# Kernel optimization log

Hardware: AMD Instinct MI355X
Metric: run time of the kernel (lower is better)

The kernel has to match this reference:

```python
import jax, jax.numpy as jnp
import numpy as np

B, N_IMG, D = 256, 128, 768
E, S, H = 3, 44, 1024  # S = ceil(128/3) rounded up to multiple of 4; H = 4*D//E
MAX_SLOTS = 88
LN_EPS = 1e-5


def setup_inputs() -> dict:
    key = jax.random.key(0)
    ks = jax.random.split(key, 12)
    x = jax.random.normal(ks[0], (B, N_IMG + 1, D), dtype=jnp.float32)
    attn_weight = jax.random.uniform(ks[1], (B, N_IMG), dtype=jnp.float32)
    ln_gamma = jnp.ones((D,), jnp.float32)
    ln_beta = jnp.zeros((D,), jnp.float32)
    vsg_w = jax.random.normal(ks[2], (D + 1, D), jnp.float32) / np.sqrt(D + 1)
    vsg_b = jnp.zeros((D,), jnp.float32)
    mu = jax.random.normal(ks[3], (E, D, MAX_SLOTS), jnp.float32) / np.sqrt(D)
    scale = jnp.ones((1,), jnp.float32)
    # per-expert MLP: kaiming-ish / xavier-ish random params
    w1 = jax.random.normal(ks[4], (E, D, H), jnp.float32) * np.sqrt(2.0 / D)
    b1 = jnp.zeros((E, H), jnp.float32)
    w2 = jax.random.normal(ks[5], (E, H, D), jnp.float32) * np.sqrt(2.0 / (H + D))
    b2 = jnp.zeros((E, D), jnp.float32)
    cw1 = jax.random.normal(ks[6], (D, 4 * D), jnp.float32) * np.sqrt(2.0 / D)
    cb1 = jnp.zeros((4 * D,), jnp.float32)
    cw2 = jax.random.normal(ks[7], (4 * D, D), jnp.float32) * np.sqrt(2.0 / (4 * D))
    cb2 = jnp.zeros((D,), jnp.float32)
    return dict(x=x, attn_weight=attn_weight, ln_gamma=ln_gamma, ln_beta=ln_beta,
                vsg_w=vsg_w, vsg_b=vsg_b, mu=mu, scale=scale,
                w1=w1, b1=b1, w2=w2, b2=b2, cw1=cw1, cb1=cb1, cw2=cw2, cb2=cb2)


def reference(x, attn_weight, ln_gamma, ln_beta, vsg_w, vsg_b, mu, scale,
              w1, b1, w2, b2, cw1, cb1, cw2, cb2):
    b, np1, d = x.shape
    n = np1 - 1
    img = x[:, 1:, :]            # [B, N, D]
    cls = x[:, 0, :]             # [B, D]

    # LayerNorm on image tokens
    mean = img.mean(-1, keepdims=True)
    var = img.var(-1, keepdims=True)  # biased, matches torch LayerNorm
    img_n = (img - mean) * jax.lax.rsqrt(var + LN_EPS) * ln_gamma + ln_beta

    # slot bias from [cls_feat, mean attention] -> visible_slot_gen (mode='original')
    attn_feat = attn_weight.mean(axis=1, keepdims=True)            # [B, 1]
    slot_input = jnp.concatenate([cls, attn_feat], axis=-1)        # [B, D+1]
    slot_bias = slot_input @ vsg_w + vsg_b                         # [B, D]

    # adjusted slot prototypes: mu[:, :, :S].permute(1,0,2) + slot_bias broadcast over (E, S)
    adj_mu = mu[:, :, :S].transpose(1, 0, 2)[None] + slot_bias[:, :, None, None]  # [B, D, E, S]

    logits = jnp.einsum('bnd,bdes->bnes', img_n * scale, adj_mu)   # [B, N, E, S]

    # expert group mask from attention thresholds (groups (1,1,1))
    vis = attn_weight > 0.7
    part = (attn_weight >= 0.3) & (attn_weight <= 0.7)
    occ = attn_weight < 0.3
    emask = jnp.stack([vis, part, occ], axis=-1).astype(logits.dtype)  # [B, N, E]
    logits = logits * emask[:, :, :, None]

    # softmax over tokens (dispatch) and over flattened slots (combine)
    dispatch = jax.nn.softmax(logits, axis=1)                      # [B, N, E, S]
    combine = jax.nn.softmax(logits.reshape(b, n, E * S), axis=-1) # [B, N, E*S]

    slot_in = jnp.einsum('bnd,bnes->besd', img, dispatch)          # [B, E, S, D]

    # batched per-expert MLP (fused grouped GEMM instead of python loop)
    h = jax.nn.gelu(jnp.einsum('besd,edh->besh', slot_in, w1) + b1[:, None, :],
                    approximate=False)
    slot_out = jnp.einsum('besh,ehd->besd', h, w2) + b2[:, None, :]  # [B, E, S, D]

    slot_flat = slot_out.reshape(b, E * S, d)
    img_out = jnp.einsum('bsd,bns->bnd', slot_flat, combine)       # [B, N, D]

    # CLS token through its dedicated dense MLP
    cls_h = jax.nn.gelu(cls @ cw1 + cb1, approximate=False)
    cls_out = cls_h @ cw2 + cb2                                    # [B, D]

    return jnp.concatenate([cls_out[:, None, :], img_out], axis=1)  # [B, N+1, D]
```

## Files before the change

kernel.cpp:

```cpp
#include <hip/hip_runtime.h>
#include <hip/hip_bf16.h>
#include <math.h>

#define NB   256
#define NIMG 128
#define DIM  768
#define NE   3
#define NS   44
#define NH   1024
#define ESL  132
#define NTOK (NB*NIMG)
#define MAXSLOTS 88
#define BIGI (1 << 30)
#define KPAD 160

typedef __bf16 bf16x8 __attribute__((ext_vector_type(8)));
typedef float f32x4 __attribute__((ext_vector_type(4)));
typedef const __attribute__((address_space(1))) void* gas_t;
typedef __attribute__((address_space(3))) void* las_t;

__device__ __forceinline__ float gelu_f(float v) {
    return 0.5f * v * (1.0f + erff(v * 0.70710678118654752f));
}

__device__ __forceinline__ float block_reduce_sum256(float v, float* red) {
    int tid = threadIdx.x;
    red[tid] = v;
    __syncthreads();
    for (int s = 128; s > 0; s >>= 1) {
        if (tid < s) red[tid] += red[tid + s];
        __syncthreads();
    }
    float r = red[0];
    __syncthreads();
    return r;
}

__global__ void repack_mu_k(const float* __restrict__ mu, __hip_bfloat16* __restrict__ bt) {
    int idx = blockIdx.x * 256 + threadIdx.x;
    if (idx >= 256 * DIM) return;
    int r = idx / DIM, d = idx - r * DIM;
    float v = 0.f;
    if (r < ESL) {
        int e = r / NS, s = r - e * NS;
        v = mu[((size_t)e * DIM + d) * MAXSLOTS + s];
    }
    bt[idx] = __float2bfloat16(v);
}

__global__ void transpose_bf16_k(const float* __restrict__ in, __hip_bfloat16* __restrict__ outp,
                                 int R, int Cc, long long inBS, long long outBS) {
    __shared__ float t[32][33];
    in   += (long long)blockIdx.z * inBS;
    outp += (long long)blockIdx.z * outBS;
    int c0 = blockIdx.x * 32, r0 = blockIdx.y * 32;
    int tx = threadIdx.x, ty = threadIdx.y;
    for (int i = 0; i < 32; i += 8) {
        int r = r0 + ty + i, c = c0 + tx;
        t[ty + i][tx] = (r < R && c < Cc) ? in[(size_t)r * Cc + c] : 0.f;
    }
    __syncthreads();
    for (int i = 0; i < 32; i += 8) {
        int r = c0 + ty + i, c = r0 + tx;
        if (r < Cc && c < R) outp[(size_t)r * R + c] = __float2bfloat16(t[tx][ty + i]);
    }
}

__global__ void cls_bf16_k(const float* __restrict__ x, __hip_bfloat16* __restrict__ cls16) {
    int idx = blockIdx.x * 256 + threadIdx.x;
    if (idx >= NB * DIM) return;
    int b = idx / DIM, j = idx - b * DIM;
    cls16[idx] = __float2bfloat16(x[(size_t)b * 129 * DIM + j]);
}

__global__ void zero_pad_k(__hip_bfloat16* __restrict__ p) {
    const int per = KPAD - ESL;
    const int total = NB * DIM * per;
    int idx = blockIdx.x * 256 + threadIdx.x;
    if (idx >= total) return;
    int bd = idx / per, k = idx - bd * per;
    p[(size_t)bd * KPAD + ESL + k] = __float2bfloat16(0.f);
}

__global__ void slot_bias_k(const float* __restrict__ x, const float* __restrict__ aw,
                            const float* __restrict__ vsg_w, const float* __restrict__ vsg_b,
                            float* __restrict__ slot_bias) {
    __shared__ float red[256];
    __shared__ float cls[DIM];
    int b = blockIdx.x, tid = threadIdx.x;
    float a = (tid < NIMG) ? aw[b * NIMG + tid] : 0.f;
    float af = block_reduce_sum256(a, red) * (1.0f / NIMG);
    for (int j = tid; j < DIM; j += 256) cls[j] = x[(size_t)b * 129 * DIM + j];
    __syncthreads();
    int j0 = tid, j1 = tid + 256, j2 = tid + 512;
    float acc0 = 0.f, acc1 = 0.f, acc2 = 0.f;
    for (int d = 0; d < DIM; ++d) {
        float c = cls[d];
        const float* wr = vsg_w + (size_t)d * DIM;
        acc0 = fmaf(c, wr[j0], acc0);
        acc1 = fmaf(c, wr[j1], acc1);
        acc2 = fmaf(c, wr[j2], acc2);
    }
    const float* wl = vsg_w + (size_t)DIM * DIM;
    float* out = slot_bias + (size_t)b * DIM;
    out[j0] = acc0 + vsg_b[j0] + af * wl[j0];
    out[j1] = acc1 + vsg_b[j1] + af * wl[j1];
    out[j2] = acc2 + vsg_b[j2] + af * wl[j2];
}

__global__ void ln_t2_k(const float* __restrict__ x, const float* __restrict__ gamma,
                        const float* __restrict__ beta, const float* __restrict__ slot_bias,
                        __hip_bfloat16* __restrict__ img_n, float* __restrict__ t2) {
    __shared__ float red[256];
    int tok = blockIdx.x;
    int b = tok >> 7, n = tok & 127;
    int tid = threadIdx.x;
    const float* row = x + ((size_t)b * 129 + 1 + n) * DIM;
    float v0 = row[tid], v1 = row[tid + 256], v2 = row[tid + 512];
    float s  = block_reduce_sum256(v0 + v1 + v2, red);
    float ss = block_reduce_sum256(v0*v0 + v1*v1 + v2*v2, red);
    float mean = s * (1.0f / DIM);
    float var  = ss * (1.0f / DIM) - mean * mean;
    float inv  = rsqrtf(var + 1e-5f);
    const float* sb = slot_bias + (size_t)b * DIM;
    __hip_bfloat16* orow = img_n + (size_t)tok * DIM;
    float tacc = 0.f;
    int j = tid;
    float y0 = (v0 - mean) * inv * gamma[j] + beta[j]; orow[j] = __float2bfloat16(y0); tacc = fmaf(y0, sb[j], tacc);
    j = tid + 256;
    float y1 = (v1 - mean) * inv * gamma[j] + beta[j]; orow[j] = __float2bfloat16(y1); tacc = fmaf(y1, sb[j], tacc);
    j = tid + 512;
    float y2 = (v2 - mean) * inv * gamma[j] + beta[j]; orow[j] = __float2bfloat16(y2); tacc = fmaf(y2, sb[j], tacc);
    float t = block_reduce_sum256(tacc, red);
    if (tid == 0) t2[tok] = t;
}

__global__ void mask_k(float* __restrict__ L, const float* __restrict__ t2,
                       const float* __restrict__ aw, const float* __restrict__ scale) {
    int idx = blockIdx.x * 256 + threadIdx.x;
    if (idx >= NTOK * ESL) return;
    int tok = idx / ESL, r = idx - tok * ESL;
    int e = r / NS;
    float a = aw[tok];
    int sel = (a > 0.7f) ? 0 : ((a >= 0.3f) ? 1 : 2);
    float v = 0.f;
    if (e == sel) v = scale[0] * (L[idx] + t2[tok]);
    L[idx] = v;
}

__global__ void dispatch_k(const float* __restrict__ L, __hip_bfloat16* __restrict__ dT16) {
    __shared__ float red[128];
    int es = blockIdx.x, b = blockIdx.y, tid = threadIdx.x;
    float v = L[((size_t)(b * NIMG + tid)) * ESL + es];
    red[tid] = v; __syncthreads();
    for (int s = 64; s > 0; s >>= 1) { if (tid < s) red[tid] = fmaxf(red[tid], red[tid + s]); __syncthreads(); }
    float mx = red[0]; __syncthreads();
    float e = __expf(v - mx);
    red[tid] = e; __syncthreads();
    for (int s = 64; s > 0; s >>= 1) { if (tid < s) red[tid] += red[tid + s]; __syncthreads(); }
    float sum = red[0];
    dT16[((size_t)b * ESL + es) * NIMG + tid] = __float2bfloat16(e / sum);
}

__global__ void combine_k(const float* __restrict__ L, __hip_bfloat16* __restrict__ C) {
    int tok = blockIdx.x, lane = threadIdx.x;
    const float* row = L + (size_t)tok * ESL;
    float v0 = row[lane], v1 = row[lane + 64];
    bool has2 = lane < (ESL - 128);
    float v2 = has2 ? row[lane + 128] : -1e30f;
    float m = fmaxf(fmaxf(v0, v1), v2);
    for (int o = 32; o > 0; o >>= 1) m = fmaxf(m, __shfl_xor(m, o));
    float e0 = __expf(v0 - m), e1 = __expf(v1 - m);
    float e2 = has2 ? __expf(v2 - m) : 0.f;
    float s = e0 + e1 + e2;
    for (int o = 32; o > 0; o >>= 1) s += __shfl_xor(s, o);
    float inv = 1.0f / s;
    __hip_bfloat16* orow = C + (size_t)tok * KPAD;
    orow[lane] = __float2bfloat16(e0 * inv);
    orow[lane + 64] = __float2bfloat16(e1 * inv);
    if (has2) orow[lane + 128] = __float2bfloat16(e2 * inv);
    else if (lane < KPAD - 128) orow[lane + 128] = __float2bfloat16(0.f);
}

__global__ __launch_bounds__(256)
void mfma2_k(const __hip_bfloat16* __restrict__ A_, long long aBS, int lda, int Mrows,
             const __hip_bfloat16* __restrict__ Bt_, long long bBS, int ldb, int Nrows,
             const float* __restrict__ bias, long long biasBS,
             void* __restrict__ Cv, long long cBS, int ldc, int cSub, long long cOuter,
             int Mlim, int Nlim, int K, int act, int out_bf16, int ctrans)
{
    const unsigned short* A  = (const unsigned short*)A_  + (long long)blockIdx.z * aBS;
    const unsigned short* Bt = (const unsigned short*)Bt_ + (long long)blockIdx.z * bBS;
    if (bias) bias += (long long)blockIdx.z * biasBS;
    long long cbase = (long long)blockIdx.z * cBS;

    __shared__ unsigned short As[128 * 32];
    __shared__ unsigned short Bs[128 * 32];

    int tid = threadIdx.x;
    int lane = tid & 63, wv = tid >> 6;
    int m0 = blockIdx.y * 128, n0 = blockIdx.x * 128;

    const unsigned short* ga[2];
    const unsigned short* gb[2];
    int ldsoff[2];
#pragma unroll
    for (int i = 0; i < 2; ++i) {
        int j = wv * 2 + i;
        int p = j * 64 + lane;
        int r = p >> 2;
        int cg = (p & 3) ^ ((r >> 1) & 3);
        int ra = m0 + r; if (ra > Mrows - 1) ra = Mrows - 1;
        int rb = n0 + r; if (rb > Nrows - 1) rb = Nrows - 1;
        ga[i] = A  + (long long)ra * lda + cg * 8;
        gb[i] = Bt + (long long)rb * ldb + cg * 8;
        ldsoff[i] = j * 512;
    }

    int lrow = lane & 15, quad = lane >> 4;
    int wm = (wv >> 1) * 64, wn = (wv & 1) * 64;
    int offA[4], offB[4];
#pragma unroll
    for (int i = 0; i < 4; ++i) {
        int rowa = wm + i * 16 + lrow;
        offA[i] = rowa * 32 + ((quad ^ ((rowa >> 1) & 3)) * 8);
        int rowb = wn + i * 16 + lrow;
        offB[i] = rowb * 32 + ((quad ^ ((rowb >> 1) & 3)) * 8);
    }

    f32x4 acc[4][4] = {};

    for (int k0 = 0; k0 < K; k0 += 32) {
        __syncthreads();
#pragma unroll
        for (int i = 0; i < 2; ++i) {
            __builtin_amdgcn_global_load_lds((gas_t)(ga[i] + k0), (las_t)(As + ldsoff[i]), 16, 0, 0);
            __builtin_amdgcn_global_load_lds((gas_t)(gb[i] + k0), (las_t)(Bs + ldsoff[i]), 16, 0, 0);
        }
        __syncthreads();
        bf16x8 af[4], bfr[4];
#pragma unroll
        for (int i = 0; i < 4; ++i) {
            af[i]  = *(const bf16x8*)(As + offA[i]);
            bfr[i] = *(const bf16x8*)(Bs + offB[i]);
        }
#pragma unroll
        for (int i = 0; i < 4; ++i)
#pragma unroll
            for (int j = 0; j < 4; ++j)
                acc[i][j] = __builtin_amdgcn_mfma_f32_16x16x32_bf16(af[i], bfr[j], acc[i][j], 0, 0, 0);
    }

    float* Cf = (float*)Cv;
    __hip_bfloat16* Cb = (__hip_bfloat16*)Cv;
    if (ctrans == 2) {
        long long cb2[4]; int cols[4];
#pragma unroll
        for (int ni = 0; ni < 4; ++ni) {
            int col = n0 + wn + ni * 16 + lrow;
            cols[ni] = col;
            int q = col / cSub, sl = col - q * cSub;
            cb2[ni] = cbase + (long long)q * cOuter + sl;
        }
#pragma unroll
        for (int mi = 0; mi < 4; ++mi) {
#pragma unroll
            for (int r = 0; r < 4; ++r) {
                int row = m0 + wm + mi * 16 + quad * 4 + r;
                if (row >= Mlim) continue;
                float bv = bias ? bias[row] : 0.f;
                long long rb = (long long)row * ldc;
#pragma unroll
                for (int ni = 0; ni < 4; ++ni) {
                    if (cols[ni] < Nlim) {
                        float v = acc[mi][ni][r] + bv;
                        if (act == 1) v = gelu_f(v);
                        long long off = cb2[ni] + rb;
                        if (out_bf16) Cb[off] = __float2bfloat16(v);
                        else          Cf[off] = v;
                    }
                }
            }
        }
    } else {
#pragma unroll
        for (int mi = 0; mi < 4; ++mi) {
#pragma unroll
            for (int r = 0; r < 4; ++r) {
                int row = m0 + wm + mi * 16 + quad * 4 + r;
                if (row >= Mlim) continue;
                int q = row / cSub;
                int sl = row - q * cSub;
                long long rb = ctrans ? (cbase + (long long)q * cOuter + sl)
                                      : (cbase + ((long long)q * cOuter + sl) * ldc);
#pragma unroll
                for (int ni = 0; ni < 4; ++ni) {
                    int col = n0 + wn + ni * 16 + lrow;
                    if (col < Nlim) {
                        float v = acc[mi][ni][r];
                        if (bias) v += bias[col];
                        if (act == 1) v = gelu_f(v);
                        long long off = ctrans ? (rb + (long long)col * ldc) : (rb + col);
                        if (out_bf16) Cb[off] = __float2bfloat16(v);
                        else          Cf[off] = v;
                    }
                }
            }
        }
    }
}

static inline void mfma2(hipStream_t st, dim3 grid,
                         const void* A, long long aBS, int lda, int Mrows,
                         const void* Bt, long long bBS, int ldb, int Nrows,
                         const float* bias, long long biasBS,
                         void* C, long long cBS, int ldc, int cSub, long long cOuter,
                         int Mlim, int Nlim, int K, int act, int obf, int ct) {
    mfma2_k<<<grid, dim3(256), 0, st>>>((const __hip_bfloat16*)A, aBS, lda, Mrows,
                                        (const __hip_bfloat16*)Bt, bBS, ldb, Nrows,
                                        bias, biasBS, C, cBS, ldc, cSub, cOuter,
                                        Mlim, Nlim, K, act, obf, ct);
}

extern "C" void kernel_launch(void* const* d_in, const int* in_sizes, int n_in,
                              void* d_out, int out_size, void* d_ws, size_t ws_size,
                              hipStream_t stream) {
    const float* x     = (const float*)d_in[0];
    const float* aw    = (const float*)d_in[1];
    const float* gamma = (const float*)d_in[2];
    const float* beta  = (const float*)d_in[3];
    const float* vsg_w = (const float*)d_in[4];
    const float* vsg_b = (const float*)d_in[5];
    const float* mu    = (const float*)d_in[6];
    const float* scale = (const float*)d_in[7];
    const float* w1    = (const float*)d_in[8];
    const float* b1    = (const float*)d_in[9];
    const float* w2    = (const float*)d_in[10];
    const float* b2    = (const float*)d_in[11];
    const float* cw1   = (const float*)d_in[12];
    const float* cb1   = (const float*)d_in[13];
    const float* cw2   = (const float*)d_in[14];
    const float* cb2   = (const float*)d_in[15];
    float* out = (float*)d_out;

    float* ws = (float*)d_ws;

    const long long IMGN_FL = (long long)NTOK * DIM / 2;
    const long long LOG_FL  = (long long)NTOK * ESL;
    const long long REG1_FL = (long long)NE * NB * NS * NH / 2;
    __hip_bfloat16* img_n = (__hip_bfloat16*)ws;
    float* logits = ws + IMGN_FL;
    __hip_bfloat16* h = (__hip_bfloat16*)ws;
    long long o = REG1_FL;
    __hip_bfloat16* dT16    = (__hip_bfloat16*)(ws + o); o += (long long)NB * ESL * NIMG / 2;
    __hip_bfloat16* comb_p  = (__hip_bfloat16*)(ws + o); o += (long long)NTOK * KPAD / 2;
    __hip_bfloat16* imgT    = (__hip_bfloat16*)(ws + o);
    __hip_bfloat16* slot_outT = imgT;                    o += (long long)NB * DIM * KPAD / 2;
    __hip_bfloat16* slot_in = (__hip_bfloat16*)(ws + o); o += (long long)NE * NB * NS * DIM / 2;
    __hip_bfloat16* mu_p    = (__hip_bfloat16*)(ws + o); o += 256 * DIM / 2;
    float* slot_bias = ws + o;                           o += NB * DIM;
    float* t2        = ws + o;                           o += NTOK;
    __hip_bfloat16* w1t  = (__hip_bfloat16*)(ws + o);    o += (long long)NE * NH * DIM / 2;
    __hip_bfloat16* w2t  = (__hip_bfloat16*)(ws + o);    o += (long long)NE * DIM * NH / 2;
    __hip_bfloat16* cw1t = (__hip_bfloat16*)(ws + o);    o += (long long)4 * DIM * DIM / 2;
    __hip_bfloat16* cw2t = (__hip_bfloat16*)(ws + o);    o += (long long)4 * DIM * DIM / 2;
    __hip_bfloat16* cls16 = (__hip_bfloat16*)(ws + o);   o += NB * DIM / 2;
    __hip_bfloat16* cls_h = (__hip_bfloat16*)(ws + o);   o += (long long)NB * 4 * DIM / 2;

    repack_mu_k<<<(256 * DIM + 255) / 256, 256, 0, stream>>>(mu, mu_p);
    transpose_bf16_k<<<dim3(NH / 32, DIM / 32, NE), dim3(32, 8), 0, stream>>>(w1, w1t, DIM, NH, (long long)DIM * NH, (long long)NH * DIM);
    transpose_bf16_k<<<dim3(DIM / 32, NH / 32, NE), dim3(32, 8), 0, stream>>>(w2, w2t, NH, DIM, (long long)NH * DIM, (long long)DIM * NH);
    transpose_bf16_k<<<dim3(4 * DIM / 32, DIM / 32, 1), dim3(32, 8), 0, stream>>>(cw1, cw1t, DIM, 4 * DIM, 0, 0);
    transpose_bf16_k<<<dim3(DIM / 32, 4 * DIM / 32, 1), dim3(32, 8), 0, stream>>>(cw2, cw2t, 4 * DIM, DIM, 0, 0);
    cls_bf16_k<<<(NB * DIM + 255) / 256, 256, 0, stream>>>(x, cls16);
    transpose_bf16_k<<<dim3(DIM / 32, NIMG / 32, NB), dim3(32, 8), 0, stream>>>(x + DIM, imgT, NIMG, DIM, (long long)129 * DIM, (long long)DIM * NIMG);

    slot_bias_k<<<NB, 256, 0, stream>>>(x, aw, vsg_w, vsg_b, slot_bias);
    ln_t2_k<<<NTOK, 256, 0, stream>>>(x, gamma, beta, slot_bias, img_n, t2);

    mfma2(stream, dim3(2, NTOK / 128, 1),
          img_n, 0, DIM, NTOK, mu_p, 0, DIM, 256, nullptr, 0,
          logits, 0, ESL, BIGI, 0, NTOK, ESL, DIM, 0, 0, 0);

    mask_k<<<(NTOK * ESL + 255) / 256, 256, 0, stream>>>(logits, t2, aw, scale);
    dispatch_k<<<dim3(ESL, NB), 128, 0, stream>>>(logits, dT16);
    combine_k<<<NTOK, 64, 0, stream>>>(logits, comb_p);

    mfma2(stream, dim3(DIM / 128, 2, NB),
          dT16, (long long)ESL * NIMG, NIMG, ESL,
          imgT, (long long)DIM * NIMG, NIMG, DIM, nullptr, 0,
          slot_in, (long long)NS * DIM, DIM, NS, NB * NS,
          ESL, DIM, NIMG, 0, 1, 0);

    mfma2(stream, dim3(NH / 128, NB * NS / 128, NE),
          slot_in, (long long)NB * NS * DIM, DIM, NB * NS,
          w1t, (long long)NH * DIM, DIM, NH, b1, NH,
          h, (long long)NB * NS * NH, NH, BIGI, 0,
          NB * NS, NH, DIM, 1, 1, 0);

    zero_pad_k<<<(NB * DIM * (KPAD - ESL) + 255) / 256, 256, 0, stream>>>(slot_outT);

    mfma2(stream, dim3(NB * NS / 128, DIM / 128, NE),
          w2t, (long long)DIM * NH, NH, DIM,
          h, (long long)NB * NS * NH, NH, NB * NS,
          b2, DIM,
          slot_outT, NS, KPAD, NS, (long long)DIM * KPAD,
          DIM, NB * NS, NH, 0, 1, 2);

    mfma2(stream, dim3(DIM / 128, 1, NB),
          comb_p, (long long)NIMG * KPAD, KPAD, NIMG,
          slot_outT, (long long)DIM * KPAD, KPAD, DIM, nullptr, 0,
          out + DIM, (long long)129 * DIM, DIM, BIGI, 0,
          NIMG, DIM, KPAD, 0, 0, 0);

    mfma2(stream, dim3(4 * DIM / 128, NB / 128, 1),
          cls16, 0, DIM, NB, cw1t, 0, DIM, 4 * DIM, cb1, 0,
          cls_h, 0, 4 * DIM, BIGI, 0, NB, 4 * DIM, DIM, 1, 1, 0);
    mfma2(stream, dim3(DIM / 128, NB / 128, 1),
          cls_h, 0, 4 * DIM, NB, cw2t, 0, 4 * DIM, DIM, cb2, 0,
          out, 0, DIM, 1, 129, NB, DIM, 4 * DIM, 0, 0, 0);
}
```

Measured before the change: 985.5 us.

## Double-buffer LDS tiles in MFMA GEMM to overlap global loads with compute

Turns the bf16 MFMA GEMM main loop into a two-stage pipeline with ping-pong LDS buffers. The next K-tile is issued via global_load_lds before the current tile's MFMAs run, and one explicit waitcnt plus barrier per iteration replaces two __syncthreads. The aim is to hide global-memory latency behind matrix math, at the cost of doubling LDS use per block (32KB), which could lower occupancy.

```diff
diff --git a/kernel.cpp b/kernel.cpp
--- a/kernel.cpp
+++ b/kernel.cpp
@@ -194,8 +194,8 @@
     if (bias) bias += (long long)blockIdx.z * biasBS;
     long long cbase = (long long)blockIdx.z * cBS;
 
-    __shared__ unsigned short As[128 * 32];
-    __shared__ unsigned short Bs[128 * 32];
+    __shared__ unsigned short As[2][128 * 32];
+    __shared__ unsigned short Bs[2][128 * 32];
 
     int tid = threadIdx.x;
     int lane = tid & 63, wv = tid >> 6;
@@ -229,26 +229,43 @@
     }
 
     f32x4 acc[4][4] = {};
-
-    for (int k0 = 0; k0 < K; k0 += 32) {
-        __syncthreads();
-#pragma unroll
-        for (int i = 0; i < 2; ++i) {
-            __builtin_amdgcn_global_load_lds((gas_t)(ga[i] + k0), (las_t)(As + ldsoff[i]), 16, 0, 0);
-            __builtin_amdgcn_global_load_lds((gas_t)(gb[i] + k0), (las_t)(Bs + ldsoff[i]), 16, 0, 0);
-        }
-        __syncthreads();
+    int nt = K >> 5;
+
+#pragma unroll
+    for (int i = 0; i < 2; ++i) {
+        __builtin_amdgcn_global_load_lds((gas_t)(ga[i]), (las_t)(&As[0][0] + ldsoff[i]), 16, 0, 0);
+        __builtin_amdgcn_global_load_lds((gas_t)(gb[i]), (las_t)(&Bs[0][0] + ldsoff[i]), 16, 0, 0);
+    }
+    asm volatile("s_waitcnt vmcnt(0)" ::: "memory");
+    __builtin_amdgcn_s_barrier();
+
+    for (int t = 0; t < nt; ++t) {
+        int cur = t & 1;
+        if (t + 1 < nt) {
+            int k0 = (t + 1) << 5;
+            int nxt = cur ^ 1;
+#pragma unroll
+            for (int i = 0; i < 2; ++i) {
+                __builtin_amdgcn_global_load_lds((gas_t)(ga[i] + k0), (las_t)(&As[nxt][0] + ldsoff[i]), 16, 0, 0);
+                __builtin_amdgcn_global_load_lds((gas_t)(gb[i] + k0), (las_t)(&Bs[nxt][0] + ldsoff[i]), 16, 0, 0);
+            }
+        }
         bf16x8 af[4], bfr[4];
 #pragma unroll
         for (int i = 0; i < 4; ++i) {
-            af[i]  = *(const bf16x8*)(As + offA[i]);
-            bfr[i] = *(const bf16x8*)(Bs + offB[i]);
+            af[i]  = *(const bf16x8*)(&As[cur][0] + offA[i]);
+            bfr[i] = *(const bf16x8*)(&Bs[cur][0] + offB[i]);
         }
 #pragma unroll
         for (int i = 0; i < 4; ++i)
 #pragma unroll
             for (int j = 0; j < 4; ++j)
                 acc[i][j] = __builtin_amdgcn_mfma_f32_16x16x32_bf16(af[i], bfr[j], acc[i][j], 0, 0, 0);
+        if (t + 1 < nt) {
+            asm volatile("s_waitcnt lgkmcnt(0)" ::: "memory");
+            asm volatile("s_waitcnt vmcnt(0)" ::: "memory");
+            __builtin_amdgcn_s_barrier();
+        }
     }
 
     float* Cf = (float*)Cv;
```

After: 950.6 us. 1.04x faster.
